# Kernel tuning notes

Hardware: AMD Instinct MI355X
Metric: run time of the kernel (lower is better)

Reference implementation:

```python
import jax, jax.numpy as jnp
import numpy as np

BIGINT = 1e10
BOA, BOH, BOL = 21, 22, 23      # global-node residue symbols
ATOM_POS_PAD = 0                # atom position pad index
AG_SEG = 1                      # antigen segment id


def setup_inputs() -> dict:
    key = jax.random.key(0)
    ks = jax.random.split(key, 8)
    B, L, C, E = 16, 128, 14, 256
    N = B * L
    # residues with global tokens at fixed positions per protein
    S = jax.random.randint(ks[0], (B, L), 0, 21)
    S = S.at[:, 0].set(BOA).at[:, 48].set(BOH).at[:, 96].set(BOL)
    S = S.reshape(N)
    seg = np.zeros((L,), np.int32); seg[0:48] = 1; seg[48:96] = 2; seg[96:] = 3
    segment_ids = jnp.tile(jnp.asarray(seg), B)
    RP = jnp.tile(jnp.arange(L, dtype=jnp.int32), B)
    A = jax.random.randint(ks[1], (N, C), 1, 16)
    AP = jax.random.randint(ks[2], (N, C), 0, 16)
    AP = AP.at[:, :4].set(jnp.arange(1, 5, dtype=AP.dtype)[None, :])  # backbone always present
    X = jax.random.normal(ks[3], (N, C, 3), dtype=jnp.float32) * 3.0
    res_embed = jax.random.normal(ks[4], (25, E), dtype=jnp.float32) * 0.02
    atom_embed = jax.random.normal(ks[5], (16, E), dtype=jnp.float32) * 0.02
    atom_pos_embed = jax.random.normal(ks[6], (16, E), dtype=jnp.float32) * 0.02
    return dict(S=S, RP=RP, A=A, AP=AP, X=X, segment_ids=segment_ids,
                res_embed=res_embed, atom_embed=atom_embed,
                atom_pos_embed=atom_pos_embed, max_n=L, k_neighbors=9)


def _embed(S, RP, A, AP, res_embed, atom_embed, atom_pos_embed):
    N = S.shape[0]
    E = res_embed.shape[1]
    half = E // 2
    inv = jnp.power(10000.0, -2.0 * jnp.arange(half, dtype=jnp.float32) / E)
    ang = RP.astype(jnp.float32)[:, None] * inv[None, :]
    pos_e = jnp.stack([jnp.sin(ang), jnp.cos(ang)], axis=-1).reshape(N, E)
    res_e = res_embed[S] + pos_e
    atom_e = atom_embed[A] + atom_pos_embed[AP]            # [N,C,E]
    not_pad = (AP != ATOM_POS_PAD)
    denom = not_pad.sum(-1, keepdims=True).astype(res_e.dtype) + 1e-10
    atom_e = jnp.sum(atom_e * not_pad[..., None], axis=1) / denom
    return jnp.concatenate([res_e, atom_e], axis=-1)       # [N,2E]


def _min_pair_dist(X, AP, max_n):
    # min over atom pairs of ||X[i,a]-X[j,b]||, pad atoms pushed to BIGINT
    N, C, _ = X.shape
    B = N // max_n
    Xb = X.reshape(B, max_n, C, 3)
    pad = (AP == ATOM_POS_PAD).reshape(B, max_n, C)
    sq = jnp.sum(Xb * Xb, axis=-1)                          # [B,L,C]
    dot = jnp.einsum('biad,bjcd->biajc', Xb, Xb)            # [B,L,C,L,C]
    d2 = sq[:, :, :, None, None] + sq[:, None, None, :, :] - 2.0 * dot
    dist = jnp.sqrt(jnp.maximum(d2, 0.0))
    pmask = pad[:, :, :, None, None] | pad[:, None, None, :, :]
    dist = dist + pmask.astype(dist.dtype) * BIGINT
    return jnp.min(dist, axis=(2, 4))                       # [B,L,L]


def _knn(dist_mat, sel_mask, k):
    # smallest-k neighbors among selected candidate edges; invalid -> -1
    B, L, _ = dist_mat.shape
    d = jnp.where(sel_mask, dist_mat, BIGINT)
    neg, dst_local = jax.lax.top_k(-d, k)                   # [B,L,k]
    valid = ((-neg) < BIGINT).reshape(-1)
    offs = (jnp.arange(B) * L)[:, None, None]
    src = jnp.broadcast_to(jnp.arange(L)[None, :, None] + offs, (B, L, k)).reshape(-1)
    dst = (dst_local + offs).reshape(-1)
    src = jnp.where(valid, src, -1)
    dst = jnp.where(valid, dst, -1)
    return jnp.stack([src, dst]), valid


def reference(S, RP, A, AP, X, segment_ids, res_embed, atom_embed, atom_pos_embed, max_n, k_neighbors):
    N = S.shape[0]
    L = max_n
    B = N // L
    h = _embed(S, RP, A, AP, res_embed, atom_embed, atom_pos_embed)
    dist = _min_pair_dist(X, AP, L)                          # [B,L,L]
    g = ((S == BOA) | (S == BOH) | (S == BOL)).reshape(B, L)
    seg = segment_ids.reshape(B, L)
    not_self = ~jnp.eye(L, dtype=bool)[None]                 # exclude i==j
    gi, gj = g[:, :, None], g[:, None, :]
    not_global = ~(gi | gj)
    same_seg = seg[:, :, None] == seg[:, None, :]
    inner_mask = same_seg & not_global & not_self
    outer_mask = (~same_seg) & not_global & not_self
    ctx_knn, ctx_valid = _knn(dist, inner_mask, k_neighbors)
    inter_knn, inter_valid = _knn(dist, outer_mask, k_neighbors)
    # non-kNN ctx edges (global_normal | global_global | sequential), dense adjacency
    global_normal = same_seg & (gi | gj) & not_self
    global_global = gi & gj & not_self
    idx = jnp.arange(L)
    adj_seq = (jnp.abs(idx[:, None] - idx[None, :]) == 1)[None]
    seq_mask = adj_seq & not_global & (seg[:, :, None] != AG_SEG)
    extra_ctx_adj = global_normal | global_global | seq_mask  # [B,L,L] bool
    return h, ctx_knn, ctx_valid, extra_ctx_adj, inter_knn, inter_valid
```

## Files before the change

### kernel.cpp

```cpp
#include <hip/hip_runtime.h>
#include <math.h>
#include <float.h>

#define BIGINT_F 1e10f
#define L_TOK 128
#define C_ATOM 14
#define E_DIM 256
#define K_NB 9

__device__ __forceinline__ float sq3(float x, float y, float z) {
    return __fadd_rn(__fadd_rn(__fmul_rn(x, x), __fmul_rn(y, y)), __fmul_rn(z, z));
}

__global__ void embed_kernel(const int* __restrict__ S, const int* __restrict__ RP,
                             const int* __restrict__ A, const int* __restrict__ AP,
                             const float* __restrict__ res_embed,
                             const float* __restrict__ atom_embed,
                             const float* __restrict__ atom_pos_embed,
                             float* __restrict__ h) {
    int n = blockIdx.x;
    int e = threadIdx.x;
    int s = S[n];
    float rp = (float)RP[n];

    int k = e >> 1;
    float invk = powf(10000.0f, -2.0f * (float)k / (float)E_DIM);
    float ang = rp * invk;
    float pe = (e & 1) ? cosf(ang) : sinf(ang);
    h[(size_t)n * (2 * E_DIM) + e] = res_embed[s * E_DIM + e] + pe;

    __shared__ int sA[C_ATOM], sAP[C_ATOM];
    if (e < C_ATOM) { sA[e] = A[n * C_ATOM + e]; sAP[e] = AP[n * C_ATOM + e]; }
    __syncthreads();

    float sum = 0.0f, cnt = 0.0f;
    for (int c = 0; c < C_ATOM; ++c) {
        if (sAP[c] != 0) {
            sum += atom_embed[sA[c] * E_DIM + e] + atom_pos_embed[sAP[c] * E_DIM + e];
            cnt += 1.0f;
        }
    }
    h[(size_t)n * (2 * E_DIM) + E_DIM + e] = sum / (cnt + 1e-10f);
}

__global__ void __launch_bounds__(L_TOK)
knn_kernel(const float* __restrict__ X, const int* __restrict__ AP,
           const int* __restrict__ S, const int* __restrict__ seg,
           float* __restrict__ ctx_src, float* __restrict__ ctx_dst, float* __restrict__ ctx_val,
           float* __restrict__ int_src, float* __restrict__ int_dst, float* __restrict__ int_val) {
    int bi = blockIdx.x;
    int b = bi >> 7;
    int i = bi & (L_TOK - 1);
    int j = threadIdx.x;
    int nj = (b << 7) + j;

    __shared__ float xi[C_ATOM][3];
    __shared__ float sqi_s[C_ATOM];
    __shared__ int   padi[C_ATOM];
    if (j < C_ATOM) {
        float x0 = X[((size_t)bi * C_ATOM + j) * 3 + 0];
        float x1 = X[((size_t)bi * C_ATOM + j) * 3 + 1];
        float x2 = X[((size_t)bi * C_ATOM + j) * 3 + 2];
        xi[j][0] = x0; xi[j][1] = x1; xi[j][2] = x2;
        sqi_s[j] = sq3(x0, x1, x2);
        padi[j] = (AP[bi * C_ATOM + j] == 0);
    }
    __syncthreads();

    float xj[C_ATOM][3], sqj[C_ATOM];
    unsigned pj = 0;
    for (int c = 0; c < C_ATOM; ++c) {
        float x0 = X[((size_t)nj * C_ATOM + c) * 3 + 0];
        float x1 = X[((size_t)nj * C_ATOM + c) * 3 + 1];
        float x2 = X[((size_t)nj * C_ATOM + c) * 3 + 2];
        xj[c][0] = x0; xj[c][1] = x1; xj[c][2] = x2;
        sqj[c] = sq3(x0, x1, x2);
        if (AP[nj * C_ATOM + c] == 0) pj |= (1u << c);
    }

    float mind2 = FLT_MAX;
    for (int a = 0; a < C_ATOM; ++a) {
        if (padi[a]) continue;
        float a0 = xi[a][0], a1 = xi[a][1], a2 = xi[a][2];
        float sa = sqi_s[a];
        for (int c = 0; c < C_ATOM; ++c) {
            if (pj & (1u << c)) continue;
            float dot = __fadd_rn(__fadd_rn(__fmul_rn(a0, xj[c][0]),
                                            __fmul_rn(a1, xj[c][1])),
                                  __fmul_rn(a2, xj[c][2]));
            float d2 = __fsub_rn(__fadd_rn(sa, sqj[c]), __fmul_rn(2.0f, dot));
            mind2 = fminf(mind2, d2);
        }
    }
    float dij = sqrtf(fmaxf(mind2, 0.0f));

    int si = S[bi], sj = S[nj];
    int segi = seg[bi], segj = seg[nj];
    bool gi = si >= 21, gj = sj >= 21;
    bool notself = (j != i);
    bool inner = (segi == segj) && !gi && !gj && notself;
    bool outer = (segi != segj) && !gi && !gj && notself;

    __shared__ float dmaster[L_TOK];
    __shared__ float dv[L_TOK];
    __shared__ int   di[L_TOK];

    for (int pass = 0; pass < 2; ++pass) {
        bool m = (pass == 0) ? inner : outer;
        float* osrc = (pass == 0) ? ctx_src : int_src;
        float* odst = (pass == 0) ? ctx_dst : int_dst;
        float* oval = (pass == 0) ? ctx_val : int_val;
        dmaster[j] = m ? dij : BIGINT_F;
        __syncthreads();
        for (int k = 0; k < K_NB; ++k) {
            dv[j] = dmaster[j];
            di[j] = j;
            __syncthreads();
            for (int s = 64; s > 0; s >>= 1) {
                if (j < s) {
                    float od = dv[j + s]; int oi = di[j + s];
                    if (od < dv[j] || (od == dv[j] && oi < di[j])) { dv[j] = od; di[j] = oi; }
                }
                __syncthreads();
            }
            if (j == 0) {
                float dmin = dv[0];
                int jmin = di[0];
                bool valid = dmin < BIGINT_F;
                int o = bi * K_NB + k;
                osrc[o] = valid ? (float)bi : -1.0f;
                odst[o] = valid ? (float)((b << 7) + jmin) : -1.0f;
                oval[o] = valid ? 1.0f : 0.0f;
                dmaster[jmin] = FLT_MAX;
            }
            __syncthreads();
        }
    }
}

__global__ void adj_kernel(const int* __restrict__ S, const int* __restrict__ seg,
                           float* __restrict__ out) {
    int idx = blockIdx.x * blockDim.x + threadIdx.x;
    int b = idx >> 14;
    int i = (idx >> 7) & (L_TOK - 1);
    int j = idx & (L_TOK - 1);
    int ni = (b << 7) + i, nj = (b << 7) + j;
    bool gi = S[ni] >= 21, gj = S[nj] >= 21;
    int segi = seg[ni], segj = seg[nj];
    bool notself = (i != j);
    bool same = (segi == segj);
    bool gn = same && (gi || gj) && notself;
    bool gg = gi && gj && notself;
    int d = i - j;
    bool adjacent = (d == 1 || d == -1);
    bool sm = adjacent && !(gi || gj) && (segi != 1);
    out[idx] = (gn || gg || sm) ? 1.0f : 0.0f;
}

extern "C" void kernel_launch(void* const* d_in, const int* in_sizes, int n_in,
                              void* d_out, int out_size, void* d_ws, size_t ws_size,
                              hipStream_t stream) {
    const int*   S    = (const int*)d_in[0];
    const int*   RP   = (const int*)d_in[1];
    const int*   A    = (const int*)d_in[2];
    const int*   AP   = (const int*)d_in[3];
    const float* X    = (const float*)d_in[4];
    const int*   seg  = (const int*)d_in[5];
    const float* rese = (const float*)d_in[6];
    const float* atme = (const float*)d_in[7];
    const float* atpe = (const float*)d_in[8];

    const int N = in_sizes[0];
    const int B = N / L_TOK;
    float* out = (float*)d_out;

    size_t off = 0;
    float* h_out = out + off;              off += (size_t)N * 2 * E_DIM;
    float* ctx_src = out + off;            off += (size_t)N * K_NB;
    float* ctx_dst = out + off;            off += (size_t)N * K_NB;
    float* ctx_val = out + off;            off += (size_t)N * K_NB;
    float* adj_out = out + off;            off += (size_t)B * L_TOK * L_TOK;
    float* int_src = out + off;            off += (size_t)N * K_NB;
    float* int_dst = out + off;            off += (size_t)N * K_NB;
    float* int_val = out + off;            off += (size_t)N * K_NB;

    embed_kernel<<<N, E_DIM, 0, stream>>>(S, RP, A, AP, rese, atme, atpe, h_out);
    knn_kernel<<<N, L_TOK, 0, stream>>>(X, AP, S, seg,
                                        ctx_src, ctx_dst, ctx_val,
                                        int_src, int_dst, int_val);
    int adj_total = B * L_TOK * L_TOK;
    adj_kernel<<<adj_total / 256, 256, 0, stream>>>(S, seg, adj_out);
}
```

Measured before the change: 119.7 us.

## Fuse embed, kNN and adjacency into one launch with wave-shuffle top-k

Merges the three kernels into a single launch whose blocks are assigned by range to the kNN, embedding or adjacency work, removing two launch overheads. The kNN part now handles one query residue per 64-lane wave with two candidates per lane, folds pad masking into an infinite squared norm, and finds each top-k element with a packed 64-bit key (distance bits plus index) reduced by shuffles instead of a shared-memory tree with many block barriers. The positional inverse frequency uses exp2f in place of powf. This adds more registers per thread and changes rounding slightly in the positional encoding.

```diff
diff --git a/kernel.cpp b/kernel.cpp
--- a/kernel.cpp
+++ b/kernel.cpp
@@ -1,6 +1,7 @@
 #include <hip/hip_runtime.h>
 #include <math.h>
 #include <float.h>
+#include <stdint.h>
 
 #define BIGINT_F 1e10f
 #define L_TOK 128
@@ -12,149 +13,163 @@
     return __fadd_rn(__fadd_rn(__fmul_rn(x, x), __fmul_rn(y, y)), __fmul_rn(z, z));
 }
 
-__global__ void embed_kernel(const int* __restrict__ S, const int* __restrict__ RP,
-                             const int* __restrict__ A, const int* __restrict__ AP,
-                             const float* __restrict__ res_embed,
-                             const float* __restrict__ atom_embed,
-                             const float* __restrict__ atom_pos_embed,
-                             float* __restrict__ h) {
-    int n = blockIdx.x;
-    int e = threadIdx.x;
-    int s = S[n];
-    float rp = (float)RP[n];
-
-    int k = e >> 1;
-    float invk = powf(10000.0f, -2.0f * (float)k / (float)E_DIM);
-    float ang = rp * invk;
-    float pe = (e & 1) ? cosf(ang) : sinf(ang);
-    h[(size_t)n * (2 * E_DIM) + e] = res_embed[s * E_DIM + e] + pe;
-
-    __shared__ int sA[C_ATOM], sAP[C_ATOM];
-    if (e < C_ATOM) { sA[e] = A[n * C_ATOM + e]; sAP[e] = AP[n * C_ATOM + e]; }
-    __syncthreads();
-
-    float sum = 0.0f, cnt = 0.0f;
-    for (int c = 0; c < C_ATOM; ++c) {
-        if (sAP[c] != 0) {
-            sum += atom_embed[sA[c] * E_DIM + e] + atom_pos_embed[sAP[c] * E_DIM + e];
-            cnt += 1.0f;
-        }
+__device__ __forceinline__ uint64_t umin64(uint64_t a, uint64_t b) { return a < b ? a : b; }
+
+__global__ void __launch_bounds__(256)
+fused_kernel(const int* __restrict__ S, const int* __restrict__ RP,
+             const int* __restrict__ A, const int* __restrict__ AP,
+             const float* __restrict__ X, const int* __restrict__ seg,
+             const float* __restrict__ res_embed,
+             const float* __restrict__ atom_embed,
+             const float* __restrict__ atom_pos_embed,
+             float* __restrict__ h,
+             float* __restrict__ ctx_src, float* __restrict__ ctx_dst, float* __restrict__ ctx_val,
+             float* __restrict__ adj_out,
+             float* __restrict__ int_src, float* __restrict__ int_dst, float* __restrict__ int_val,
+             int N) {
+    const int NKNN = N / 4;
+    int blk = blockIdx.x;
+    int tid = threadIdx.x;
+
+    if (blk < NKNN) {
+        int wave = tid >> 6;
+        int lane = tid & 63;
+        int bi = blk * 4 + wave;
+        int b  = bi >> 7;
+        int i  = bi & (L_TOK - 1);
+
+        __shared__ float4 sxi[4][C_ATOM];
+        if (lane < C_ATOM) {
+            const float* xp = X + ((size_t)bi * C_ATOM + lane) * 3;
+            float x0 = xp[0], x1 = xp[1], x2 = xp[2];
+            float sq = (AP[bi * C_ATOM + lane] == 0) ? INFINITY : sq3(x0, x1, x2);
+            sxi[wave][lane] = make_float4(x0, x1, x2, sq);
+        }
+        __syncthreads();
+
+        float xa0[C_ATOM], xa1[C_ATOM], xa2[C_ATOM], sa[C_ATOM];
+        #pragma unroll
+        for (int a = 0; a < C_ATOM; ++a) {
+            float4 t = sxi[wave][a];
+            xa0[a] = t.x; xa1[a] = t.y; xa2[a] = t.z; sa[a] = t.w;
+        }
+
+        int j0 = lane, j1 = lane + 64;
+        int nj0 = (b << 7) + j0, nj1 = (b << 7) + j1;
+
+        float mind0 = INFINITY, mind1 = INFINITY;
+        for (int c = 0; c < C_ATOM; ++c) {
+            const float* yp0 = X + ((size_t)nj0 * C_ATOM + c) * 3;
+            const float* yp1 = X + ((size_t)nj1 * C_ATOM + c) * 3;
+            float y00 = yp0[0], y01 = yp0[1], y02 = yp0[2];
+            float y10 = yp1[0], y11 = yp1[1], y12 = yp1[2];
+            float sc0 = (AP[nj0 * C_ATOM + c] == 0) ? INFINITY : sq3(y00, y01, y02);
+            float sc1 = (AP[nj1 * C_ATOM + c] == 0) ? INFINITY : sq3(y10, y11, y12);
+            #pragma unroll
+            for (int a = 0; a < C_ATOM; ++a) {
+                float dot0 = __fadd_rn(__fadd_rn(__fmul_rn(xa0[a], y00),
+                                                 __fmul_rn(xa1[a], y01)),
+                                       __fmul_rn(xa2[a], y02));
+                float d20 = __fsub_rn(__fadd_rn(sa[a], sc0), __fmul_rn(2.0f, dot0));
+                mind0 = fminf(mind0, d20);
+                float dot1 = __fadd_rn(__fadd_rn(__fmul_rn(xa0[a], y10),
+                                                 __fmul_rn(xa1[a], y11)),
+                                       __fmul_rn(xa2[a], y12));
+                float d21 = __fsub_rn(__fadd_rn(sa[a], sc1), __fmul_rn(2.0f, dot1));
+                mind1 = fminf(mind1, d21);
+            }
+        }
+        float d0 = sqrtf(fmaxf(mind0, 0.0f));
+        float d1 = sqrtf(fmaxf(mind1, 0.0f));
+
+        int si = S[bi];
+        int segi = seg[bi];
+        bool gi = si >= 21;
+        int sj0 = S[nj0], sj1 = S[nj1];
+        int segj0 = seg[nj0], segj1 = seg[nj1];
+        bool gj0 = sj0 >= 21, gj1 = sj1 >= 21;
+        bool ng0 = !gi && !gj0 && (j0 != i);
+        bool ng1 = !gi && !gj1 && (j1 != i);
+        bool inner0 = (segi == segj0) && ng0;
+        bool inner1 = (segi == segj1) && ng1;
+        bool outer0 = (segi != segj0) && ng0;
+        bool outer1 = (segi != segj1) && ng1;
+
+        const uint32_t bigbits = __float_as_uint(BIGINT_F);
+        uint64_t kd0 = ((uint64_t)__float_as_uint(d0) << 32) | (uint32_t)j0;
+        uint64_t kd1 = ((uint64_t)__float_as_uint(d1) << 32) | (uint32_t)j1;
+        uint64_t kbig0 = ((uint64_t)bigbits << 32) | (uint32_t)j0;
+        uint64_t kbig1 = ((uint64_t)bigbits << 32) | (uint32_t)j1;
+
+        for (int pass = 0; pass < 2; ++pass) {
+            uint64_t k0 = (pass == 0 ? inner0 : outer0) ? kd0 : kbig0;
+            uint64_t k1 = (pass == 0 ? inner1 : outer1) ? kd1 : kbig1;
+            float* osrc = (pass == 0) ? ctx_src : int_src;
+            float* odst = (pass == 0) ? ctx_dst : int_dst;
+            float* oval = (pass == 0) ? ctx_val : int_val;
+            #pragma unroll
+            for (int k = 0; k < K_NB; ++k) {
+                uint64_t kk = umin64(k0, k1);
+                #pragma unroll
+                for (int m = 32; m > 0; m >>= 1) {
+                    uint64_t o = __shfl_xor((unsigned long long)kk, m, 64);
+                    kk = umin64(kk, o);
+                }
+                if (k0 == kk) k0 = UINT64_MAX;
+                if (k1 == kk) k1 = UINT64_MAX;
+                if (lane == 0) {
+                    uint32_t dbits = (uint32_t)(kk >> 32);
+                    int jmin = (int)(uint32_t)kk;
+                    bool valid = dbits < bigbits;
+                    int o = bi * K_NB + k;
+                    osrc[o] = valid ? (float)bi : -1.0f;
+                    odst[o] = valid ? (float)((b << 7) + jmin) : -1.0f;
+                    oval[o] = valid ? 1.0f : 0.0f;
+                }
+            }
+        }
+    } else if (blk < NKNN + N) {
+        int n = blk - NKNN;
+        int e = tid;
+        int s = S[n];
+        float rp = (float)RP[n];
+
+        int k = e >> 1;
+        const float c1 = (float)(-2.0 * 13.287712379549449 / (double)E_DIM);
+        float invk = exp2f((float)k * c1);
+        float ang = rp * invk;
+        float pe = (e & 1) ? cosf(ang) : sinf(ang);
+        h[(size_t)n * (2 * E_DIM) + e] = res_embed[s * E_DIM + e] + pe;
+
+        __shared__ int sA[C_ATOM], sAP[C_ATOM];
+        if (e < C_ATOM) { sA[e] = A[n * C_ATOM + e]; sAP[e] = AP[n * C_ATOM + e]; }
+        __syncthreads();
+
+        float sum = 0.0f, cnt = 0.0f;
+        for (int c = 0; c < C_ATOM; ++c) {
+            if (sAP[c] != 0) {
+                sum += atom_embed[sA[c] * E_DIM + e] + atom_pos_embed[sAP[c] * E_DIM + e];
+                cnt += 1.0f;
+            }
+        }
+        h[(size_t)n * (2 * E_DIM) + E_DIM + e] = sum / (cnt + 1e-10f);
+    } else {
+        int idx = (blk - NKNN - N) * 256 + tid;
+        int b = idx >> 14;
+        int i = (idx >> 7) & (L_TOK - 1);
+        int j = idx & (L_TOK - 1);
+        int ni = (b << 7) + i, nj = (b << 7) + j;
+        bool gi = S[ni] >= 21, gj = S[nj] >= 21;
+        int segi = seg[ni], segj = seg[nj];
+        bool notself = (i != j);
+        bool same = (segi == segj);
+        bool gn = same && (gi || gj) && notself;
+        bool gg = gi && gj && notself;
+        int d = i - j;
+        bool adjacent = (d == 1 || d == -1);
+        bool sm = adjacent && !(gi || gj) && (segi != 1);
+        adj_out[idx] = (gn || gg || sm) ? 1.0f : 0.0f;
     }
-    h[(size_t)n * (2 * E_DIM) + E_DIM + e] = sum / (cnt + 1e-10f);
-}
-
-__global__ void __launch_bounds__(L_TOK)
-knn_kernel(const float* __restrict__ X, const int* __restrict__ AP,
-           const int* __restrict__ S, const int* __restrict__ seg,
-           float* __restrict__ ctx_src, float* __restrict__ ctx_dst, float* __restrict__ ctx_val,
-           float* __restrict__ int_src, float* __restrict__ int_dst, float* __restrict__ int_val) {
-    int bi = blockIdx.x;
-    int b = bi >> 7;
-    int i = bi & (L_TOK - 1);
-    int j = threadIdx.x;
-    int nj = (b << 7) + j;
-
-    __shared__ float xi[C_ATOM][3];
-    __shared__ float sqi_s[C_ATOM];
-    __shared__ int   padi[C_ATOM];
-    if (j < C_ATOM) {
-        float x0 = X[((size_t)bi * C_ATOM + j) * 3 + 0];
-        float x1 = X[((size_t)bi * C_ATOM + j) * 3 + 1];
-        float x2 = X[((size_t)bi * C_ATOM + j) * 3 + 2];
-        xi[j][0] = x0; xi[j][1] = x1; xi[j][2] = x2;
-        sqi_s[j] = sq3(x0, x1, x2);
-        padi[j] = (AP[bi * C_ATOM + j] == 0);
-    }
-    __syncthreads();
-
-    float xj[C_ATOM][3], sqj[C_ATOM];
-    unsigned pj = 0;
-    for (int c = 0; c < C_ATOM; ++c) {
-        float x0 = X[((size_t)nj * C_ATOM + c) * 3 + 0];
-        float x1 = X[((size_t)nj * C_ATOM + c) * 3 + 1];
-        float x2 = X[((size_t)nj * C_ATOM + c) * 3 + 2];
-        xj[c][0] = x0; xj[c][1] = x1; xj[c][2] = x2;
-        sqj[c] = sq3(x0, x1, x2);
-        if (AP[nj * C_ATOM + c] == 0) pj |= (1u << c);
-    }
-
-    float mind2 = FLT_MAX;
-    for (int a = 0; a < C_ATOM; ++a) {
-        if (padi[a]) continue;
-        float a0 = xi[a][0], a1 = xi[a][1], a2 = xi[a][2];
-        float sa = sqi_s[a];
-        for (int c = 0; c < C_ATOM; ++c) {
-            if (pj & (1u << c)) continue;
-            float dot = __fadd_rn(__fadd_rn(__fmul_rn(a0, xj[c][0]),
-                                            __fmul_rn(a1, xj[c][1])),
-                                  __fmul_rn(a2, xj[c][2]));
-            float d2 = __fsub_rn(__fadd_rn(sa, sqj[c]), __fmul_rn(2.0f, dot));
-            mind2 = fminf(mind2, d2);
-        }
-    }
-    float dij = sqrtf(fmaxf(mind2, 0.0f));
-
-    int si = S[bi], sj = S[nj];
-    int segi = seg[bi], segj = seg[nj];
-    bool gi = si >= 21, gj = sj >= 21;
-    bool notself = (j != i);
-    bool inner = (segi == segj) && !gi && !gj && notself;
-    bool outer = (segi != segj) && !gi && !gj && notself;
-
-    __shared__ float dmaster[L_TOK];
-    __shared__ float dv[L_TOK];
-    __shared__ int   di[L_TOK];
-
-    for (int pass = 0; pass < 2; ++pass) {
-        bool m = (pass == 0) ? inner : outer;
-        float* osrc = (pass == 0) ? ctx_src : int_src;
-        float* odst = (pass == 0) ? ctx_dst : int_dst;
-        float* oval = (pass == 0) ? ctx_val : int_val;
-        dmaster[j] = m ? dij : BIGINT_F;
-        __syncthreads();
-        for (int k = 0; k < K_NB; ++k) {
-            dv[j] = dmaster[j];
-            di[j] = j;
-            __syncthreads();
-            for (int s = 64; s > 0; s >>= 1) {
-                if (j < s) {
-                    float od = dv[j + s]; int oi = di[j + s];
-                    if (od < dv[j] || (od == dv[j] && oi < di[j])) { dv[j] = od; di[j] = oi; }
-                }
-                __syncthreads();
-            }
-            if (j == 0) {
-                float dmin = dv[0];
-                int jmin = di[0];
-                bool valid = dmin < BIGINT_F;
-                int o = bi * K_NB + k;
-                osrc[o] = valid ? (float)bi : -1.0f;
-                odst[o] = valid ? (float)((b << 7) + jmin) : -1.0f;
-                oval[o] = valid ? 1.0f : 0.0f;
-                dmaster[jmin] = FLT_MAX;
-            }
-            __syncthreads();
-        }
-    }
-}
-
-__global__ void adj_kernel(const int* __restrict__ S, const int* __restrict__ seg,
-                           float* __restrict__ out) {
-    int idx = blockIdx.x * blockDim.x + threadIdx.x;
-    int b = idx >> 14;
-    int i = (idx >> 7) & (L_TOK - 1);
-    int j = idx & (L_TOK - 1);
-    int ni = (b << 7) + i, nj = (b << 7) + j;
-    bool gi = S[ni] >= 21, gj = S[nj] >= 21;
-    int segi = seg[ni], segj = seg[nj];
-    bool notself = (i != j);
-    bool same = (segi == segj);
-    bool gn = same && (gi || gj) && notself;
-    bool gg = gi && gj && notself;
-    int d = i - j;
-    bool adjacent = (d == 1 || d == -1);
-    bool sm = adjacent && !(gi || gj) && (segi != 1);
-    out[idx] = (gn || gg || sm) ? 1.0f : 0.0f;
 }
 
 extern "C" void kernel_launch(void* const* d_in, const int* in_sizes, int n_in,
@@ -175,19 +190,19 @@
     float* out = (float*)d_out;
 
     size_t off = 0;
-    float* h_out = out + off;              off += (size_t)N * 2 * E_DIM;
-    float* ctx_src = out + off;            off += (size_t)N * K_NB;
-    float* ctx_dst = out + off;            off += (size_t)N * K_NB;
-    float* ctx_val = out + off;            off += (size_t)N * K_NB;
-    float* adj_out = out + off;            off += (size_t)B * L_TOK * L_TOK;
-    float* int_src = out + off;            off += (size_t)N * K_NB;
-    float* int_dst = out + off;            off += (size_t)N * K_NB;
-    float* int_val = out + off;            off += (size_t)N * K_NB;
-
-    embed_kernel<<<N, E_DIM, 0, stream>>>(S, RP, A, AP, rese, atme, atpe, h_out);
-    knn_kernel<<<N, L_TOK, 0, stream>>>(X, AP, S, seg,
-                                        ctx_src, ctx_dst, ctx_val,
-                                        int_src, int_dst, int_val);
-    int adj_total = B * L_TOK * L_TOK;
-    adj_kernel<<<adj_total / 256, 256, 0, stream>>>(S, seg, adj_out);
+    float* h_out   = out + off;  off += (size_t)N * 2 * E_DIM;
+    float* ctx_src = out + off;  off += (size_t)N * K_NB;
+    float* ctx_dst = out + off;  off += (size_t)N * K_NB;
+    float* ctx_val = out + off;  off += (size_t)N * K_NB;
+    float* adj_out = out + off;  off += (size_t)B * L_TOK * L_TOK;
+    float* int_src = out + off;  off += (size_t)N * K_NB;
+    float* int_dst = out + off;  off += (size_t)N * K_NB;
+    float* int_val = out + off;  off += (size_t)N * K_NB;
+
+    int nknn = N / 4;
+    int nadj = (B * L_TOK * L_TOK) / 256;
+    int grid = nknn + N + nadj;
+    fused_kernel<<<grid, 256, 0, stream>>>(S, RP, A, AP, X, seg, rese, atme, atpe,
+                                           h_out, ctx_src, ctx_dst, ctx_val,
+                                           adj_out, int_src, int_dst, int_val, N);
 }
```

After: 97.45 us. 1.23x faster.
